# Performance work log

Measured on AMD Instinct MI355X. Metric: run time of the kernel, lower is better.

## Reference

```python
import jax, jax.numpy as jnp
import numpy as np

MODES = (16, 16, 16)  # (kx, ky, kz); rfft keeps kz//2+1 = 9 modes on last axis


def setup_inputs() -> dict:
    key = jax.random.key(0)
    k_x, k_w1, k_w2 = jax.random.split(key, 3)
    B, C, H, W, D = 4, 64, 64, 64, 64
    hidden = C // 4
    kzr = MODES[2] // 2 + 1
    gate_dim = MODES[0] * MODES[1] * kzr  # 16*16*9 = 2304
    x = jax.random.normal(k_x, (B, C, H, W, D), dtype=jnp.float32)
    w1 = jax.random.normal(k_w1, (C, hidden), dtype=jnp.float32) * (1.0 / np.sqrt(C))
    b1 = jnp.zeros((hidden,), dtype=jnp.float32)
    w2 = jax.random.normal(k_w2, (hidden, gate_dim), dtype=jnp.float32) * (1.0 / np.sqrt(hidden))
    b2 = jnp.zeros((gate_dim,), dtype=jnp.float32)
    return {"x": x, "w1": w1, "b1": b1, "w2": w2, "b2": b2}


def reference(x, w1, b1, w2, b2):
    B = x.shape[0]
    kx, ky, kz = MODES
    kzr = kz // 2 + 1
    # Gate network: global average pool over spatial dims -> MLP -> sigmoid
    pooled = jnp.mean(x, axis=(2, 3, 4))                      # [B, C]
    h = jax.nn.relu(pooled @ w1 + b1)                          # [B, C//4]
    gates = jax.nn.sigmoid(h @ w2 + b2)                        # [B, kx*ky*kzr]
    gates = gates.reshape(B, 1, kx, ky, kzr)                   # broadcast over channels
    # Full 3D rFFT, gate only the low-frequency corner block, inverse FFT
    x_ft = jnp.fft.rfftn(x, axes=(-3, -2, -1))                 # [B, C, H, W, D//2+1] complex
    x_ft_gated = x_ft.at[:, :, :kx, :ky, :kzr].multiply(gates.astype(x_ft.real.dtype))
    out = jnp.fft.irfftn(x_ft_gated, s=x.shape[-3:], axes=(-3, -2, -1))
    return out.astype(x.dtype)
```

## Files before the change

kernel.cpp:

```cpp
#include <hip/hip_runtime.h>

namespace {

constexpr float COS64[64] = {
  1.00000000f,  0.99518473f,  0.98078528f,  0.95694034f,
  0.92387953f,  0.88192126f,  0.83146961f,  0.77301045f,
  0.70710678f,  0.63439328f,  0.55557023f,  0.47139674f,
  0.38268343f,  0.29028468f,  0.19509032f,  0.09801714f,
  0.00000000f, -0.09801714f, -0.19509032f, -0.29028468f,
 -0.38268343f, -0.47139674f, -0.55557023f, -0.63439328f,
 -0.70710678f, -0.77301045f, -0.83146961f, -0.88192126f,
 -0.92387953f, -0.95694034f, -0.98078528f, -0.99518473f,
 -1.00000000f, -0.99518473f, -0.98078528f, -0.95694034f,
 -0.92387953f, -0.88192126f, -0.83146961f, -0.77301045f,
 -0.70710678f, -0.63439328f, -0.55557023f, -0.47139674f,
 -0.38268343f, -0.29028468f, -0.19509032f, -0.09801714f,
 -0.00000000f,  0.09801714f,  0.19509032f,  0.29028468f,
  0.38268343f,  0.47139674f,  0.55557023f,  0.63439328f,
  0.70710678f,  0.77301045f,  0.83146961f,  0.88192126f,
  0.92387953f,  0.95694034f,  0.98078528f,  0.99518473f };

constexpr float C16[16] = {
  1.00000000f,  0.92387953f,  0.70710678f,  0.38268343f,
  0.00000000f, -0.38268343f, -0.70710678f, -0.92387953f,
 -1.00000000f, -0.92387953f, -0.70710678f, -0.38268343f,
 -0.00000000f,  0.38268343f,  0.70710678f,  0.92387953f };

constexpr float TWOPI_64 = 0.09817477042468103f;
constexpr int MM = 144;
constexpr int GD = 2304;
constexpr int ZW = 576;

__global__ __launch_bounds__(256) void k1_fwd(const float* __restrict__ x,
                                              float2* __restrict__ buf1) {
  __shared__ float xs[64 * 68];
  const int tid = threadIdx.x;
  const int slice = blockIdx.x;
  const int w = tid >> 2, q = tid & 3;

  const float4* xp = (const float4*)(x + ((size_t)slice << 12));
  const float4 a0 = xp[tid];
  const float4 a1 = xp[tid + 256];
  const float4 a2 = xp[tid + 512];
  const float4 a3 = xp[tid + 768];
  {
    const int s0 = tid & 15, hi = tid >> 4;
    *(float4*)&xs[(hi +  0) * 68 + s0 * 4] = a0;
    *(float4*)&xs[(hi + 16) * 68 + s0 * 4] = a1;
    *(float4*)&xs[(hi + 32) * 68 + s0 * 4] = a2;
    *(float4*)&xs[(hi + 48) * 68 + s0 * 4] = a3;
  }
  __syncthreads();

  float xv[16];
  {
    const float4 b0 = *(const float4*)&xs[w * 68 + q * 16 + 0];
    const float4 b1 = *(const float4*)&xs[w * 68 + q * 16 + 4];
    const float4 b2 = *(const float4*)&xs[w * 68 + q * 16 + 8];
    const float4 b3 = *(const float4*)&xs[w * 68 + q * 16 + 12];
    xv[0]=b0.x; xv[1]=b0.y; xv[2]=b0.z; xv[3]=b0.w;
    xv[4]=b1.x; xv[5]=b1.y; xv[6]=b1.z; xv[7]=b1.w;
    xv[8]=b2.x; xv[9]=b2.y; xv[10]=b2.z; xv[11]=b2.w;
    xv[12]=b3.x; xv[13]=b3.y; xv[14]=b3.z; xv[15]=b3.w;
  }

  float ar[9], ai[9];
#pragma unroll
  for (int kz = 0; kz < 9; ++kz) { ar[kz] = 0.f; ai[kz] = 0.f; }
#pragma unroll
  for (int j = 0; j < 16; ++j) {
    const float v = xv[j];
#pragma unroll
    for (int kz = 0; kz < 9; ++kz) {
      const int n = (kz * j) & 63;
      ar[kz] = fmaf(v, COS64[n], ar[kz]);
      ai[kz] = fmaf(v, -COS64[(n + 48) & 63], ai[kz]);
    }
  }
  float2* bp = buf1 + (size_t)slice * ZW;
#pragma unroll
  for (int kz = 0; kz < 9; ++kz) {
    const int m = (q * kz) & 3;
    const float a = ar[kz], b = ai[kz];
    float r  = (m & 1) ? b : a;
    float i2 = (m & 1) ? a : b;
    r  = (m >= 2) ? -r : r;
    i2 = (m == 1 || m == 2) ? -i2 : i2;
    r  += __shfl_xor(r, 1);  r  += __shfl_xor(r, 2);
    i2 += __shfl_xor(i2, 1); i2 += __shfl_xor(i2, 2);
    if (q == 0) bp[kz * 64 + w] = make_float2(r, i2);
  }
}

__global__ __launch_bounds__(256) void k2_fwd(const float2* __restrict__ buf1,
                                              float2* __restrict__ buf2) {
  __shared__ float2 As[64 * 64];
  __shared__ float2 Bs[64 * 17];
  const int tid = threadIdx.x;
  const int kz = blockIdx.x, bc = blockIdx.y;

  {
    const int wl = tid & 63, hb = tid >> 6;
#pragma unroll
    for (int i = 0; i < 16; ++i) {
      const int h = hb + 4 * i;
      As[h * 64 + (wl ^ (h & 31))] =
          buf1[((size_t)bc * 64 + h) * ZW + kz * 64 + wl];
    }
  }
  __syncthreads();

  const int h = tid & 63, kyg = tid >> 6;
  float bR[4] = {0.f, 0.f, 0.f, 0.f}, bI[4] = {0.f, 0.f, 0.f, 0.f};
  {
    const float sc = COS64[kyg];
    const float ss = COS64[(kyg + 48) & 63];
    float pR = 1.f, pI = 0.f;
    const int hl = h & 31;
    const float2* Ah = As + h * 64;
    for (int w1 = 0; w1 < 4; ++w1) {
#pragma unroll
      for (int w0 = 0; w0 < 16; ++w0) {
        const int w = w1 * 16 + w0;
        const float2 a = Ah[w ^ hl];
        const float tR = a.x * pR - a.y * pI;
        const float tI = a.x * pI + a.y * pR;
        bR[0] += tR; bI[0] += tI;
#pragma unroll
        for (int j = 1; j < 4; ++j) {
          const int n = (j * w0) & 15;
          const float c = C16[n], s = C16[(n + 12) & 15];
          bR[j] = fmaf(tR, c, fmaf(tI, s, bR[j]));
          bI[j] = fmaf(tI, c, fmaf(-tR, s, bI[j]));
        }
        const float nR = fmaf(pR, sc, pI * ss);
        const float nI = fmaf(pI, sc, -pR * ss);
        pR = nR; pI = nI;
      }
    }
  }
#pragma unroll
  for (int j = 0; j < 4; ++j)
    Bs[h * 17 + kyg + 4 * j] = make_float2(bR[j], bI[j]);
  __syncthreads();

  {
    const int kx = tid >> 4, ky = tid & 15;
    const float hc = COS64[kx];
    const float hs = COS64[(kx + 48) & 63];
    float qR = 1.f, qI = 0.f, sR = 0.f, sI = 0.f;
    for (int h2 = 0; h2 < 64; ++h2) {
      const float2 b = Bs[h2 * 17 + ky];
      sR = fmaf(b.x, qR, fmaf(-b.y, qI, sR));
      sI = fmaf(b.x, qI, fmaf( b.y, qR, sI));
      const float nR = fmaf(qR, hc, qI * hs);
      const float nI = fmaf(qI, hc, -qR * hs);
      qR = nR; qI = nI;
    }
    buf2[(size_t)bc * GD + kx * MM + ky * 9 + kz] = make_float2(sR, sI);
  }
}

__global__ __launch_bounds__(256) void k3_gates(const float2* __restrict__ buf2,
    const float* __restrict__ w1, const float* __restrict__ b1,
    const float* __restrict__ w2, const float* __restrict__ b2,
    float* __restrict__ gm1) {
  __shared__ float pooled[64];
  __shared__ float hs[16];
  const int b = blockIdx.x, tid = threadIdx.x;
  if (tid < 64)
    pooled[tid] = buf2[(size_t)(b * 64 + tid) * GD].x * (1.f / 262144.f);
  __syncthreads();
  if (tid < 16) {
    float acc = b1[tid];
    for (int c = 0; c < 64; ++c) acc = fmaf(pooled[c], w1[c * 16 + tid], acc);
    hs[tid] = fmaxf(acc, 0.f);
  }
  __syncthreads();
#pragma unroll
  for (int r = 0; r < 9; ++r) {
    const int o = tid + r * 256;
    float acc = b2[o];
#pragma unroll
    for (int j = 0; j < 16; ++j) acc = fmaf(hs[j], w2[j * GD + o], acc);
    gm1[b * GD + o] = 1.f / (1.f + expf(-acc)) - 1.f;
  }
}

__global__ __launch_bounds__(256) void k4b_final(const float2* __restrict__ S,
                                                 const float* __restrict__ gm1,
                                                 const float* __restrict__ x,
                                                 float* __restrict__ out) {
  __shared__ float2 C1s[MM];
  __shared__ float2 C2s[9 * 65];
  __shared__ float deltaS[64 * 68];
  const int tid = threadIdx.x, slice = blockIdx.x;
  const int bc = slice >> 6, h = slice & 63, b = bc >> 6;
  const int w = tid >> 2, q = tid & 3;

  const float4* xp = (const float4*)(x + ((size_t)slice << 12));
  const float4 xv0 = xp[tid];
  const float4 xv1 = xp[tid + 256];
  const float4 xv2 = xp[tid + 512];
  const float4 xv3 = xp[tid + 768];

  if (tid < MM) {
    const float2* Sp = S + (size_t)bc * GD + tid;
    const float* Gp = gm1 + (size_t)b * GD + tid;
    float sn, cs;
    sincosf(TWOPI_64 * (float)h, &sn, &cs);
    float px = 1.f, py = 0.f, ar = 0.f, ai = 0.f;
#pragma unroll
    for (int kx = 0; kx < 16; ++kx) {
      const float2 sv = Sp[kx * MM];
      const float g = Gp[kx * MM];
      const float dR = sv.x * g, dI = sv.y * g;
      ar = fmaf(dR, px, fmaf(-dI, py, ar));
      ai = fmaf(dR, py, fmaf( dI, px, ai));
      const float nx = fmaf(px, cs, -py * sn);
      const float ny = fmaf(px, sn,  py * cs);
      px = nx; py = ny;
    }
    C1s[tid] = make_float2(ar, ai);
  }
  __syncthreads();

  {
    float sn, cs;
    sincosf(TWOPI_64 * (float)w, &sn, &cs);
    const int kz0 = q, kz1 = q + 4;
    float a0r = 0.f, a0i = 0.f, a1r = 0.f, a1i = 0.f, a2r = 0.f, a2i = 0.f;
    float px = 1.f, py = 0.f;
    for (int ky = 0; ky < 16; ++ky) {
      const float2 c0 = C1s[ky * 9 + kz0];
      const float2 c1 = C1s[ky * 9 + kz1];
      a0r = fmaf(c0.x, px, fmaf(-c0.y, py, a0r));
      a0i = fmaf(c0.x, py, fmaf( c0.y, px, a0i));
      a1r = fmaf(c1.x, px, fmaf(-c1.y, py, a1r));
      a1i = fmaf(c1.x, py, fmaf( c1.y, px, a1i));
      if (q == 0) {
        const float2 c2v = C1s[ky * 9 + 8];
        a2r = fmaf(c2v.x, px, fmaf(-c2v.y, py, a2r));
        a2i = fmaf(c2v.x, py, fmaf( c2v.y, px, a2i));
      }
      const float nx = fmaf(px, cs, -py * sn);
      const float ny = fmaf(px, sn,  py * cs);
      px = nx; py = ny;
    }
    C2s[kz0 * 65 + w] = make_float2(a0r, a0i);
    C2s[kz1 * 65 + w] = make_float2(a1r, a1i);
    if (q == 0) C2s[8 * 65 + w] = make_float2(a2r, a2i);
  }
  __syncthreads();

  {
    float cr[9], ci[9];
#pragma unroll
    for (int kz = 0; kz < 9; ++kz) {
      const float2 v = C2s[kz * 65 + w];
      const int m = (kz * q) & 3;
      const float a = v.x, b2_ = v.y;
      float r  = (m & 1) ? b2_ : a;
      float i2 = (m & 1) ? a : b2_;
      r  = (m == 1 || m == 2) ? -r : r;
      i2 = (m >= 2) ? -i2 : i2;
      cr[kz] = r; ci[kz] = i2;
    }
    float acc[16];
#pragma unroll
    for (int j = 0; j < 16; ++j) acc[j] = cr[0];
#pragma unroll
    for (int kz = 1; kz < 9; ++kz) {
#pragma unroll
      for (int j = 0; j < 16; ++j) {
        const int n = (kz * j) & 63;
        acc[j] = fmaf(cr[kz],  2.f * COS64[n], acc[j]);
        acc[j] = fmaf(ci[kz], -2.f * COS64[(n + 48) & 63], acc[j]);
      }
    }
    const float scale = 1.f / 262144.f;
    float4 d0, d1, d2, d3;
    d0.x = acc[0]  * scale; d0.y = acc[1]  * scale;
    d0.z = acc[2]  * scale; d0.w = acc[3]  * scale;
    d1.x = acc[4]  * scale; d1.y = acc[5]  * scale;
    d1.z = acc[6]  * scale; d1.w = acc[7]  * scale;
    d2.x = acc[8]  * scale; d2.y = acc[9]  * scale;
    d2.z = acc[10] * scale; d2.w = acc[11] * scale;
    d3.x = acc[12] * scale; d3.y = acc[13] * scale;
    d3.z = acc[14] * scale; d3.w = acc[15] * scale;
    *(float4*)&deltaS[w * 68 + q * 16 + 0]  = d0;
    *(float4*)&deltaS[w * 68 + q * 16 + 4]  = d1;
    *(float4*)&deltaS[w * 68 + q * 16 + 8]  = d2;
    *(float4*)&deltaS[w * 68 + q * 16 + 12] = d3;
  }
  __syncthreads();

  {
    const int s0 = tid & 15, hi = tid >> 4;
    const float4 r0 = *(const float4*)&deltaS[(hi +  0) * 68 + s0 * 4];
    const float4 r1 = *(const float4*)&deltaS[(hi + 16) * 68 + s0 * 4];
    const float4 r2 = *(const float4*)&deltaS[(hi + 32) * 68 + s0 * 4];
    const float4 r3 = *(const float4*)&deltaS[(hi + 48) * 68 + s0 * 4];
    float4* op = (float4*)(out + ((size_t)slice << 12));
    float4 o0 = xv0, o1 = xv1, o2 = xv2, o3 = xv3;
    o0.x += r0.x; o0.y += r0.y; o0.z += r0.z; o0.w += r0.w;
    o1.x += r1.x; o1.y += r1.y; o1.z += r1.z; o1.w += r1.w;
    o2.x += r2.x; o2.y += r2.y; o2.z += r2.z; o2.w += r2.w;
    o3.x += r3.x; o3.y += r3.y; o3.z += r3.z; o3.w += r3.w;
    op[tid]       = o0;
    op[tid + 256] = o1;
    op[tid + 512] = o2;
    op[tid + 768] = o3;
  }
}

}

extern "C" void kernel_launch(void* const* d_in, const int* in_sizes, int n_in,
                              void* d_out, int out_size, void* d_ws, size_t ws_size,
                              hipStream_t stream) {
  (void)in_sizes; (void)n_in; (void)out_size; (void)ws_size;
  const float* x  = (const float*)d_in[0];
  const float* w1 = (const float*)d_in[1];
  const float* b1 = (const float*)d_in[2];
  const float* w2 = (const float*)d_in[3];
  const float* b2 = (const float*)d_in[4];
  float* out = (float*)d_out;

  char* ws = (char*)d_ws;
  float2* buf1 = (float2*)ws;
  float2* buf2 = (float2*)(ws + 75497472);
  float*  gm1  = (float*)(ws + 75497472 + 4718592);

  hipLaunchKernelGGL(k1_fwd,   dim3(16384),    dim3(256), 0, stream, x, buf1);
  hipLaunchKernelGGL(k2_fwd,   dim3(9, 256),   dim3(256), 0, stream, buf1, buf2);
  hipLaunchKernelGGL(k3_gates, dim3(4),        dim3(256), 0, stream, buf2, w1, b1, w2, b2, gm1);
  hipLaunchKernelGGL(k4b_final,dim3(16384),    dim3(256), 0, stream, buf2, gm1, x, out);
}
```

Measured before the change: 256.1 us.

## Fuse W-axis DFT into first kernel and shrink intermediate buffer

The first kernel now performs the W-axis truncated DFT (16 ky modes) in shared memory right after the D-axis DFT. It writes only 144 complex values per slice instead of 576, which cuts the intermediate global traffic by about four times. The second kernel then does only the H-axis DFT, with one block per (b,c) staging data through shared memory in two chunks. The cost is extra serial work per slice in k1, where only 144 of 256 threads run a 64-step loop, and far fewer blocks in k2 (256 instead of 2304).

```diff
diff --git a/kernel.cpp b/kernel.cpp
--- a/kernel.cpp
+++ b/kernel.cpp
@@ -20,20 +20,14 @@
   0.70710678f,  0.77301045f,  0.83146961f,  0.88192126f,
   0.92387953f,  0.95694034f,  0.98078528f,  0.99518473f };
 
-constexpr float C16[16] = {
-  1.00000000f,  0.92387953f,  0.70710678f,  0.38268343f,
-  0.00000000f, -0.38268343f, -0.70710678f, -0.92387953f,
- -1.00000000f, -0.92387953f, -0.70710678f, -0.38268343f,
- -0.00000000f,  0.38268343f,  0.70710678f,  0.92387953f };
-
 constexpr float TWOPI_64 = 0.09817477042468103f;
 constexpr int MM = 144;
 constexpr int GD = 2304;
-constexpr int ZW = 576;
 
 __global__ __launch_bounds__(256) void k1_fwd(const float* __restrict__ x,
                                               float2* __restrict__ buf1) {
   __shared__ float xs[64 * 68];
+  __shared__ float2 As[9 * 67];
   const int tid = threadIdx.x;
   const int slice = blockIdx.x;
   const int w = tid >> 2, q = tid & 3;
@@ -77,7 +71,6 @@
       ai[kz] = fmaf(v, -COS64[(n + 48) & 63], ai[kz]);
     }
   }
-  float2* bp = buf1 + (size_t)slice * ZW;
 #pragma unroll
   for (int kz = 0; kz < 9; ++kz) {
     const int m = (q * kz) & 3;
@@ -88,77 +81,61 @@
     i2 = (m == 1 || m == 2) ? -i2 : i2;
     r  += __shfl_xor(r, 1);  r  += __shfl_xor(r, 2);
     i2 += __shfl_xor(i2, 1); i2 += __shfl_xor(i2, 2);
-    if (q == 0) bp[kz * 64 + w] = make_float2(r, i2);
+    if (q == 0) As[kz * 67 + w] = make_float2(r, i2);
+  }
+  __syncthreads();
+
+  if (tid < MM) {
+    const int ky = tid / 9, kz = tid - ky * 9;
+    const float cs = COS64[ky], sn = COS64[(ky + 48) & 63];
+    float px = 1.f, py = 0.f, br = 0.f, bi = 0.f;
+    for (int ww = 0; ww < 64; ++ww) {
+      const float2 a = As[kz * 67 + ww];
+      br = fmaf(a.x, px, fmaf(-a.y, py, br));
+      bi = fmaf(a.x, py, fmaf( a.y, px, bi));
+      const float nx = fmaf(px, cs,  py * sn);
+      const float ny = fmaf(py, cs, -px * sn);
+      px = nx; py = ny;
+    }
+    buf1[(size_t)slice * MM + tid] = make_float2(br, bi);
   }
 }
 
 __global__ __launch_bounds__(256) void k2_fwd(const float2* __restrict__ buf1,
                                               float2* __restrict__ buf2) {
-  __shared__ float2 As[64 * 64];
-  __shared__ float2 Bs[64 * 17];
-  const int tid = threadIdx.x;
-  const int kz = blockIdx.x, bc = blockIdx.y;
-
-  {
-    const int wl = tid & 63, hb = tid >> 6;
-#pragma unroll
-    for (int i = 0; i < 16; ++i) {
-      const int h = hb + 4 * i;
-      As[h * 64 + (wl ^ (h & 31))] =
-          buf1[((size_t)bc * 64 + h) * ZW + kz * 64 + wl];
-    }
-  }
-  __syncthreads();
-
-  const int h = tid & 63, kyg = tid >> 6;
-  float bR[4] = {0.f, 0.f, 0.f, 0.f}, bI[4] = {0.f, 0.f, 0.f, 0.f};
-  {
-    const float sc = COS64[kyg];
-    const float ss = COS64[(kyg + 48) & 63];
-    float pR = 1.f, pI = 0.f;
-    const int hl = h & 31;
-    const float2* Ah = As + h * 64;
-    for (int w1 = 0; w1 < 4; ++w1) {
-#pragma unroll
-      for (int w0 = 0; w0 < 16; ++w0) {
-        const int w = w1 * 16 + w0;
-        const float2 a = Ah[w ^ hl];
-        const float tR = a.x * pR - a.y * pI;
-        const float tI = a.x * pI + a.y * pR;
-        bR[0] += tR; bI[0] += tI;
-#pragma unroll
-        for (int j = 1; j < 4; ++j) {
-          const int n = (j * w0) & 15;
-          const float c = C16[n], s = C16[(n + 12) & 15];
-          bR[j] = fmaf(tR, c, fmaf(tI, s, bR[j]));
-          bI[j] = fmaf(tI, c, fmaf(-tR, s, bI[j]));
-        }
-        const float nR = fmaf(pR, sc, pI * ss);
-        const float nI = fmaf(pI, sc, -pR * ss);
-        pR = nR; pI = nI;
+  __shared__ float2 Bs[32 * MM];
+  const int tid = threadIdx.x, bc = blockIdx.x;
+  const int kx = tid >> 4, g = tid & 15;
+
+  float accR[9], accI[9];
+#pragma unroll
+  for (int j = 0; j < 9; ++j) { accR[j] = 0.f; accI[j] = 0.f; }
+  float qR = 1.f, qI = 0.f;
+  const float hc = COS64[kx], hsn = COS64[(kx + 48) & 63];
+
+  const float4* src = (const float4*)(buf1 + (size_t)bc * 64 * MM);
+  for (int c2 = 0; c2 < 2; ++c2) {
+    float4* dst4 = (float4*)Bs;
+    for (int i = tid; i < 2304; i += 256) dst4[i] = src[c2 * 2304 + i];
+    __syncthreads();
+    for (int hh = 0; hh < 32; ++hh) {
+      const float2* row = Bs + hh * MM + g * 9;
+#pragma unroll
+      for (int j = 0; j < 9; ++j) {
+        const float2 b = row[j];
+        accR[j] = fmaf(b.x, qR, fmaf(-b.y, qI, accR[j]));
+        accI[j] = fmaf(b.x, qI, fmaf( b.y, qR, accI[j]));
       }
-    }
-  }
-#pragma unroll
-  for (int j = 0; j < 4; ++j)
-    Bs[h * 17 + kyg + 4 * j] = make_float2(bR[j], bI[j]);
-  __syncthreads();
-
-  {
-    const int kx = tid >> 4, ky = tid & 15;
-    const float hc = COS64[kx];
-    const float hs = COS64[(kx + 48) & 63];
-    float qR = 1.f, qI = 0.f, sR = 0.f, sI = 0.f;
-    for (int h2 = 0; h2 < 64; ++h2) {
-      const float2 b = Bs[h2 * 17 + ky];
-      sR = fmaf(b.x, qR, fmaf(-b.y, qI, sR));
-      sI = fmaf(b.x, qI, fmaf( b.y, qR, sI));
-      const float nR = fmaf(qR, hc, qI * hs);
-      const float nI = fmaf(qI, hc, -qR * hs);
+      const float nR = fmaf(qR, hc, qI * hsn);
+      const float nI = fmaf(qI, hc, -qR * hsn);
       qR = nR; qI = nI;
     }
-    buf2[(size_t)bc * GD + kx * MM + ky * 9 + kz] = make_float2(sR, sI);
-  }
+    __syncthreads();
+  }
+
+  float2* dst = buf2 + (size_t)bc * GD + kx * MM + g * 9;
+#pragma unroll
+  for (int j = 0; j < 9; ++j) dst[j] = make_float2(accR[j], accI[j]);
 }
 
 __global__ __launch_bounds__(256) void k3_gates(const float2* __restrict__ buf2,
@@ -329,11 +306,11 @@
 
   char* ws = (char*)d_ws;
   float2* buf1 = (float2*)ws;
-  float2* buf2 = (float2*)(ws + 75497472);
-  float*  gm1  = (float*)(ws + 75497472 + 4718592);
+  float2* buf2 = (float2*)(ws + 18874368);
+  float*  gm1  = (float*)(ws + 18874368 + 4718592);
 
   hipLaunchKernelGGL(k1_fwd,   dim3(16384),    dim3(256), 0, stream, x, buf1);
-  hipLaunchKernelGGL(k2_fwd,   dim3(9, 256),   dim3(256), 0, stream, buf1, buf2);
+  hipLaunchKernelGGL(k2_fwd,   dim3(256),      dim3(256), 0, stream, buf1, buf2);
   hipLaunchKernelGGL(k3_gates, dim3(4),        dim3(256), 0, stream, buf2, w1, b1, w2, b2, gm1);
   hipLaunchKernelGGL(k4b_final,dim3(16384),    dim3(256), 0, stream, buf2, gm1, x, out);
 }
```

Result: faster. 250.9 us (-2.0%).
